# Kernel tuning notes

Measured on AMD Instinct MI355X. Metric: run time of the kernel, lower is better.

Reference implementation:

```python
import jax, jax.numpy as jnp
import numpy as np

BN_EPS = 1e-3  # Keras BatchNormalization default epsilon

def setup_inputs() -> dict:
    key = jax.random.key(0)
    ks = jax.random.split(key, 6)
    B, H, W, C = 8, 128, 128, 128
    s = 0.05  # small init scale for weights
    return {
        "x1": jax.random.normal(ks[0], (B, H, W, C), jnp.float32),
        "x2": jax.random.normal(ks[1], (B, H, W, C), jnp.float32),
        "Wq": jax.random.normal(ks[2], (C, C), jnp.float32) * s,
        "Wk": jax.random.normal(ks[3], (C, C), jnp.float32) * s,
        "Wv": jax.random.normal(ks[4], (C, C), jnp.float32) * s,
        "Ws": jax.random.normal(ks[5], (C, C), jnp.float32) * s,
        "bs": jnp.zeros((C,), jnp.float32),
        "scale": jnp.ones((1,), jnp.float32),   # layers.Attention use_scale=True, init 1
        "gamma": jnp.ones((C,), jnp.float32),
        "beta": jnp.zeros((C,), jnp.float32),
        "mu": jnp.zeros((C,), jnp.float32),
        "var": jnp.ones((C,), jnp.float32),
    }


def reference(x1, x2, Wq, Wk, Wv, Ws, bs, scale, gamma, beta, mu, var):
    # x1, x2: [B,H,W,C].  1x1 convs with relu == per-pixel channel matmul.
    q = jax.nn.relu(jnp.einsum('bhwc,cd->bhwd', x1, Wq))  # [B,H,W,C]
    k = jax.nn.relu(jnp.einsum('bhwc,cd->bhwd', x1, Wk))
    v = jax.nn.relu(jnp.einsum('bhwc,cd->bhwd', x2, Wv))
    # After transpose [0,3,1,2], Keras Attention batches over (B,C):
    # seq axis = H (rows), feature dim = W (cols). Fold the transposes into einsum.
    scores = scale[0] * jnp.einsum('bhwc,bgwc->bchg', q, k)  # [B,C,H,H]
    attn = jax.nn.softmax(scores, axis=-1)
    # attn @ v over row axis g, then implicit transpose back to NHWC.
    o = jnp.einsum('bchg,bgwc->bhwc', attn, v)  # [B,H,W,C]
    # sigmoid 1x1 conv (with bias), then inference-mode BatchNorm.
    g = jax.nn.sigmoid(jnp.einsum('bhwc,cd->bhwd', o, Ws) + bs)
    g = gamma * (g - mu) * jax.lax.rsqrt(var + BN_EPS) + beta
    # gated residual
    return x1 + x2 * g
```

## Files before the change

### kernel.cpp

```cpp
#include <hip/hip_runtime.h>

typedef unsigned int u32;
typedef unsigned short u16;
typedef u16 u16x4 __attribute__((ext_vector_type(4)));
typedef u16 u16x8 __attribute__((ext_vector_type(8)));
typedef __bf16 bf16x8 __attribute__((ext_vector_type(8)));
typedef float f32x4 __attribute__((ext_vector_type(4)));

#define LDK 136
#define MFMA(a, b, c) __builtin_amdgcn_mfma_f32_16x16x32_bf16(a, b, c, 0, 0, 0)

__device__ __forceinline__ u16 f2b(float f) {
  u32 u = __builtin_bit_cast(u32, f);
  u = (u + 0x7fffu + ((u >> 16) & 1u)) >> 16;
  return (u16)u;
}
__device__ __forceinline__ float b2f(u16 h) {
  u32 u = ((u32)h) << 16;
  return __builtin_bit_cast(float, u);
}

__global__ void wprep(const float* __restrict__ Wq, const float* __restrict__ Wk,
                      const float* __restrict__ Wv, const float* __restrict__ Ws,
                      u16* __restrict__ wT) {
  const float* srcs[4] = {Wq, Wk, Wv, Ws};
  const float* s = srcs[blockIdx.x];
  u16* d = wT + (size_t)blockIdx.x * 16384;
  for (int idx = threadIdx.x; idx < 16384; idx += 256) {
    int i = idx >> 7, j = idx & 127;
    d[j * 128 + i] = f2b(s[idx]);
  }
}

__global__ __launch_bounds__(256, 2)
void qkv_kernel(const float* __restrict__ x1, const float* __restrict__ x2,
                const u16* __restrict__ wT,
                u16* __restrict__ q_t, u16* __restrict__ k_t, u16* __restrict__ v_t) {
  __shared__ u16 Xs[128 * LDK];
  __shared__ u16 ST[128 * LDK];

  const int t = threadIdx.x;
  const int bh = blockIdx.x;
  const int b = bh >> 7, h = bh & 127;
  const size_t pixbase = (size_t)bh * 16384;
  const size_t obase = (size_t)b * 2097152 + (size_t)h * 128;

#pragma unroll
  for (int j = 0; j < 8; ++j) {
    int lin = j * 256 + t;
    int w = lin >> 4, c0 = (lin & 15) << 3;
    f32x4 a0 = *(const f32x4*)&x1[pixbase + lin * 8];
    f32x4 a1 = *(const f32x4*)&x1[pixbase + lin * 8 + 4];
    u16x8 p;
#pragma unroll
    for (int i = 0; i < 4; ++i) { p[i] = f2b(a0[i]); p[4 + i] = f2b(a1[i]); }
    *(u16x8*)&Xs[w * LDK + c0] = p;
  }
  __syncthreads();

  const int lane = t & 63, wave = t >> 6;
  const int lrow = lane & 15, lq = lane >> 4;
  const int nstrip = wave * 32;

  u16* outs[3] = {q_t, k_t, v_t};

  for (int m = 0; m < 3; ++m) {
    const u16* wb = wT + (size_t)m * 16384;
    bf16x8 w0[4], w1[4];
#pragma unroll
    for (int kk = 0; kk < 4; ++kk) {
      int ko = kk * 32 + lq * 8;
      w0[kk] = *(const bf16x8*)&wb[(nstrip + lrow) * 128 + ko];
      w1[kk] = *(const bf16x8*)&wb[(nstrip + 16 + lrow) * 128 + ko];
    }

    if (m == 2) {
#pragma unroll
      for (int j = 0; j < 8; ++j) {
        int lin = j * 256 + t;
        int w = lin >> 4, c0 = (lin & 15) << 3;
        f32x4 a0 = *(const f32x4*)&x2[pixbase + lin * 8];
        f32x4 a1 = *(const f32x4*)&x2[pixbase + lin * 8 + 4];
        u16x8 p;
#pragma unroll
        for (int i = 0; i < 4; ++i) { p[i] = f2b(a0[i]); p[4 + i] = f2b(a1[i]); }
        *(u16x8*)&Xs[w * LDK + c0] = p;
      }
      __syncthreads();
    }

    f32x4 acc[8][2];
#pragma unroll
    for (int mt = 0; mt < 8; ++mt) {
      acc[mt][0] = (f32x4){0.f, 0.f, 0.f, 0.f};
      acc[mt][1] = (f32x4){0.f, 0.f, 0.f, 0.f};
    }
#pragma unroll
    for (int kk = 0; kk < 4; ++kk) {
      int ko = kk * 32 + lq * 8;
#pragma unroll
      for (int mt = 0; mt < 8; ++mt) {
        bf16x8 a = *(const bf16x8*)&Xs[(mt * 16 + lrow) * LDK + ko];
        acc[mt][0] = MFMA(a, w0[kk], acc[mt][0]);
        acc[mt][1] = MFMA(a, w1[kk], acc[mt][1]);
      }
    }
    __syncthreads();

#pragma unroll
    for (int mt = 0; mt < 8; ++mt) {
      int w0i = mt * 16 + lq * 4;
#pragma unroll
      for (int nt = 0; nt < 2; ++nt) {
        int c = nstrip + nt * 16 + lrow;
        u16x4 p;
#pragma unroll
        for (int r = 0; r < 4; ++r) p[r] = f2b(fmaxf(acc[mt][nt][r], 0.f));
        *(u16x4*)&ST[c * LDK + w0i] = p;
      }
    }
    __syncthreads();

    u16* dst = outs[m];
    {
      int c = t >> 1, w0i = (t & 1) * 64;
#pragma unroll
      for (int j = 0; j < 8; ++j)
        *(u16x8*)&dst[obase + (size_t)c * 16384 + w0i + j * 8] =
            *(const u16x8*)&ST[c * LDK + w0i + j * 8];
    }
  }
}

__global__ __launch_bounds__(256, 2)
void attn_kernel(u16* __restrict__ q_t, const u16* __restrict__ k_t,
                 const u16* __restrict__ v_t, const float* __restrict__ scale_p) {
  __shared__ u16 Ks[128 * LDK];
  __shared__ u16 QP[128 * LDK];

  const int t = threadIdx.x;
  const size_t base = (size_t)blockIdx.x * 16384;

#pragma unroll
  for (int j = 0; j < 8; ++j) {
    int lin = j * 256 + t;
    int r = lin >> 4, c0 = (lin & 15) << 3;
    *(u16x8*)&QP[r * LDK + c0] = *(const u16x8*)&q_t[base + lin * 8];
    *(u16x8*)&Ks[r * LDK + c0] = *(const u16x8*)&k_t[base + lin * 8];
  }
  __syncthreads();

  const int lane = t & 63, wave = t >> 6;
  const int lrow = lane & 15, lq = lane >> 4;
  const int hstrip = wave * 32;
  const float scl = scale_p[0];

  f32x4 acc[8][2];
#pragma unroll
  for (int mt = 0; mt < 8; ++mt) {
    acc[mt][0] = (f32x4){0.f, 0.f, 0.f, 0.f};
    acc[mt][1] = (f32x4){0.f, 0.f, 0.f, 0.f};
  }
#pragma unroll
  for (int kk = 0; kk < 4; ++kk) {
    int ko = kk * 32 + lq * 8;
    bf16x8 b0 = *(const bf16x8*)&QP[(hstrip + lrow) * LDK + ko];
    bf16x8 b1 = *(const bf16x8*)&QP[(hstrip + 16 + lrow) * LDK + ko];
#pragma unroll
    for (int mt = 0; mt < 8; ++mt) {
      bf16x8 a = *(const bf16x8*)&Ks[(mt * 16 + lrow) * LDK + ko];
      acc[mt][0] = MFMA(a, b0, acc[mt][0]);
      acc[mt][1] = MFMA(a, b1, acc[mt][1]);
    }
  }

  const int g0 = (t & 15) * 8, w0v = (t >> 4) * 8;
  u16x8 vv[8];
#pragma unroll
  for (int i = 0; i < 8; ++i)
    vv[i] = *(const u16x8*)&v_t[base + (g0 + i) * 128 + w0v];

  float inv[2];
#pragma unroll
  for (int nt = 0; nt < 2; ++nt) {
    float mx = -1e30f;
#pragma unroll
    for (int mt = 0; mt < 8; ++mt)
#pragma unroll
      for (int r = 0; r < 4; ++r) {
        acc[mt][nt][r] *= scl;
        mx = fmaxf(mx, acc[mt][nt][r]);
      }
    mx = fmaxf(mx, __shfl_xor(mx, 16));
    mx = fmaxf(mx, __shfl_xor(mx, 32));
    float s = 0.f;
#pragma unroll
    for (int mt = 0; mt < 8; ++mt)
#pragma unroll
      for (int r = 0; r < 4; ++r) {
        float e = __expf(acc[mt][nt][r] - mx);
        acc[mt][nt][r] = e;
        s += e;
      }
    s += __shfl_xor(s, 16);
    s += __shfl_xor(s, 32);
    inv[nt] = 1.f / s;
  }
  __syncthreads();

#pragma unroll
  for (int j = 0; j < 8; ++j) {
    u16x8 tv;
#pragma unroll
    for (int i = 0; i < 8; ++i) tv[i] = vv[i][j];
    *(u16x8*)&Ks[(w0v + j) * LDK + g0] = tv;
  }
#pragma unroll
  for (int mt = 0; mt < 8; ++mt) {
    int gg0 = mt * 16 + lq * 4;
#pragma unroll
    for (int nt = 0; nt < 2; ++nt) {
      int hh = hstrip + nt * 16 + lrow;
      u16x4 p;
#pragma unroll
      for (int r = 0; r < 4; ++r) p[r] = f2b(acc[mt][nt][r] * inv[nt]);
      *(u16x4*)&QP[hh * LDK + gg0] = p;
    }
  }
  __syncthreads();

  f32x4 o[8][2];
#pragma unroll
  for (int mt = 0; mt < 8; ++mt) {
    o[mt][0] = (f32x4){0.f, 0.f, 0.f, 0.f};
    o[mt][1] = (f32x4){0.f, 0.f, 0.f, 0.f};
  }
#pragma unroll
  for (int kk = 0; kk < 4; ++kk) {
    int ko = kk * 32 + lq * 8;
    bf16x8 b0 = *(const bf16x8*)&QP[(hstrip + lrow) * LDK + ko];
    bf16x8 b1 = *(const bf16x8*)&QP[(hstrip + 16 + lrow) * LDK + ko];
#pragma unroll
    for (int mt = 0; mt < 8; ++mt) {
      bf16x8 a = *(const bf16x8*)&Ks[(mt * 16 + lrow) * LDK + ko];
      o[mt][0] = MFMA(a, b0, o[mt][0]);
      o[mt][1] = MFMA(a, b1, o[mt][1]);
    }
  }
  __syncthreads();

#pragma unroll
  for (int mt = 0; mt < 8; ++mt) {
    int w0i = mt * 16 + lq * 4;
#pragma unroll
    for (int nt = 0; nt < 2; ++nt) {
      int hh = hstrip + nt * 16 + lrow;
      u16x4 p;
#pragma unroll
      for (int r = 0; r < 4; ++r) p[r] = f2b(o[mt][nt][r]);
      *(u16x4*)&Ks[hh * LDK + w0i] = p;
    }
  }
  __syncthreads();

  {
    int hh = t >> 1, w0i = (t & 1) * 64;
#pragma unroll
    for (int j = 0; j < 8; ++j)
      *(u16x8*)&q_t[base + hh * 128 + w0i + j * 8] =
          *(const u16x8*)&Ks[hh * LDK + w0i + j * 8];
  }
}

__global__ __launch_bounds__(256, 3)
void final_kernel(const u16* __restrict__ o_t, const u16* __restrict__ wsT,
                  const float* __restrict__ x1, const float* __restrict__ x2,
                  const float* __restrict__ bs, const float* __restrict__ gamma,
                  const float* __restrict__ beta, const float* __restrict__ mu,
                  const float* __restrict__ var, float* __restrict__ out) {
  __shared__ u16 Os[128 * LDK];
  __shared__ float bnA[128], bnB[128], bsf[128];

  const int t = threadIdx.x;
  const int bh = blockIdx.x;
  const int b = bh >> 7, h = bh & 127;
  const size_t obase = (size_t)b * 2097152 + (size_t)h * 128;
  const size_t pixbase = (size_t)bh * 16384;

  if (t < 128) {
    float a = gamma[t] * rsqrtf(var[t] + 1e-3f);
    bnA[t] = a;
    bnB[t] = beta[t] - mu[t] * a;
    bsf[t] = bs[t];
  }
  {
    int c0 = (t & 15) * 8, w0 = (t >> 4) * 8;
    u16 ov[8][8];
#pragma unroll
    for (int i = 0; i < 8; ++i)
      *(u16x8*)&ov[i][0] = *(const u16x8*)&o_t[obase + (size_t)(c0 + i) * 16384 + w0];
#pragma unroll
    for (int j = 0; j < 8; ++j) {
      u16x8 tv;
#pragma unroll
      for (int i = 0; i < 8; ++i) tv[i] = ov[i][j];
      *(u16x8*)&Os[(w0 + j) * LDK + c0] = tv;
    }
  }
  __syncthreads();

  const int lane = t & 63, wave = t >> 6;
  const int lrow = lane & 15, lq = lane >> 4;
  const int wstrip = wave * 32;

  f32x4 acc[8][2];
#pragma unroll
  for (int mt = 0; mt < 8; ++mt) {
    acc[mt][0] = (f32x4){0.f, 0.f, 0.f, 0.f};
    acc[mt][1] = (f32x4){0.f, 0.f, 0.f, 0.f};
  }
#pragma unroll
  for (int kk = 0; kk < 4; ++kk) {
    int ko = kk * 32 + lq * 8;
    bf16x8 b0 = *(const bf16x8*)&Os[(wstrip + lrow) * LDK + ko];
    bf16x8 b1 = *(const bf16x8*)&Os[(wstrip + 16 + lrow) * LDK + ko];
#pragma unroll
    for (int mt = 0; mt < 8; ++mt) {
      bf16x8 a = *(const bf16x8*)&wsT[(mt * 16 + lrow) * 128 + ko];
      acc[mt][0] = MFMA(a, b0, acc[mt][0]);
      acc[mt][1] = MFMA(a, b1, acc[mt][1]);
    }
  }
  __syncthreads();

#pragma unroll
  for (int mt = 0; mt < 8; ++mt) {
    int d0 = mt * 16 + lq * 4;
#pragma unroll
    for (int nt = 0; nt < 2; ++nt) {
      int w = wstrip + nt * 16 + lrow;
      u16x4 p;
#pragma unroll
      for (int r = 0; r < 4; ++r) {
        int d = d0 + r;
        float sv = acc[mt][nt][r] + bsf[d];
        float sg = 1.f / (1.f + __expf(-sv));
        p[r] = f2b(bnA[d] * sg + bnB[d]);
      }
      *(u16x4*)&Os[w * LDK + d0] = p;
    }
  }
  __syncthreads();

  {
    int w = t >> 1, d0 = (t & 1) * 64;
#pragma unroll
    for (int j = 0; j < 8; ++j) {
      int d = d0 + j * 8;
      u16x8 g8 = *(const u16x8*)&Os[w * LDK + d];
      f32x4 a0 = *(const f32x4*)&x1[pixbase + w * 128 + d];
      f32x4 a1 = *(const f32x4*)&x1[pixbase + w * 128 + d + 4];
      f32x4 c0v = *(const f32x4*)&x2[pixbase + w * 128 + d];
      f32x4 c1v = *(const f32x4*)&x2[pixbase + w * 128 + d + 4];
      f32x4 r0, r1;
#pragma unroll
      for (int i = 0; i < 4; ++i) {
        r0[i] = a0[i] + c0v[i] * b2f(g8[i]);
        r1[i] = a1[i] + c1v[i] * b2f(g8[4 + i]);
      }
      *(f32x4*)&out[pixbase + w * 128 + d] = r0;
      *(f32x4*)&out[pixbase + w * 128 + d + 4] = r1;
    }
  }
}

extern "C" void kernel_launch(void* const* d_in, const int* in_sizes, int n_in,
                              void* d_out, int out_size, void* d_ws, size_t ws_size,
                              hipStream_t stream) {
  const float* x1 = (const float*)d_in[0];
  const float* x2 = (const float*)d_in[1];
  const float* Wq = (const float*)d_in[2];
  const float* Wk = (const float*)d_in[3];
  const float* Wv = (const float*)d_in[4];
  const float* Ws = (const float*)d_in[5];
  const float* bs = (const float*)d_in[6];
  const float* scale = (const float*)d_in[7];
  const float* gamma = (const float*)d_in[8];
  const float* beta = (const float*)d_in[9];
  const float* mu = (const float*)d_in[10];
  const float* var = (const float*)d_in[11];
  float* outp = (float*)d_out;

  u16* q_t = (u16*)d_ws;
  u16* k_t = q_t + 16777216;
  u16* v_t = k_t + 16777216;
  u16* wT = v_t + 16777216;

  wprep<<<dim3(4), dim3(256), 0, stream>>>(Wq, Wk, Wv, Ws, wT);
  qkv_kernel<<<dim3(1024), dim3(256), 0, stream>>>(x1, x2, wT, q_t, k_t, v_t);
  attn_kernel<<<dim3(1024), dim3(256), 0, stream>>>(q_t, k_t, v_t, scale);
  final_kernel<<<dim3(1024), dim3(256), 0, stream>>>(q_t, wT + 3 * 16384, x1, x2, bs,
                                                     gamma, beta, mu, var, outp);
}
```

Baseline: 360.9 us.

## Split QKV projection across grid Y and cut shared-memory staging in attention

```diff
diff --git a/kernel.cpp b/kernel.cpp
--- a/kernel.cpp
+++ b/kernel.cpp
@@ -32,25 +32,41 @@
   }
 }
 
-__global__ __launch_bounds__(256, 2)
+__global__ __launch_bounds__(256, 4)
 void qkv_kernel(const float* __restrict__ x1, const float* __restrict__ x2,
                 const u16* __restrict__ wT,
                 u16* __restrict__ q_t, u16* __restrict__ k_t, u16* __restrict__ v_t) {
   __shared__ u16 Xs[128 * LDK];
-  __shared__ u16 ST[128 * LDK];
 
   const int t = threadIdx.x;
   const int bh = blockIdx.x;
+  const int m = blockIdx.y;
   const int b = bh >> 7, h = bh & 127;
   const size_t pixbase = (size_t)bh * 16384;
   const size_t obase = (size_t)b * 2097152 + (size_t)h * 128;
 
+  const float* xin = (m == 2) ? x2 : x1;
+  u16* dst = (m == 0) ? q_t : (m == 1) ? k_t : v_t;
+
+  const int lane = t & 63, wave = t >> 6;
+  const int lrow = lane & 15, lq = lane >> 4;
+  const int nstrip = wave * 32;
+
+  const u16* wb = wT + (size_t)m * 16384;
+  bf16x8 w0[4], w1[4];
+#pragma unroll
+  for (int kk = 0; kk < 4; ++kk) {
+    int ko = kk * 32 + lq * 8;
+    w0[kk] = *(const bf16x8*)&wb[(nstrip + lrow) * 128 + ko];
+    w1[kk] = *(const bf16x8*)&wb[(nstrip + 16 + lrow) * 128 + ko];
+  }
+
 #pragma unroll
   for (int j = 0; j < 8; ++j) {
     int lin = j * 256 + t;
     int w = lin >> 4, c0 = (lin & 15) << 3;
-    f32x4 a0 = *(const f32x4*)&x1[pixbase + lin * 8];
-    f32x4 a1 = *(const f32x4*)&x1[pixbase + lin * 8 + 4];
+    f32x4 a0 = *(const f32x4*)&xin[pixbase + lin * 8];
+    f32x4 a1 = *(const f32x4*)&xin[pixbase + lin * 8 + 4];
     u16x8 p;
 #pragma unroll
     for (int i = 0; i < 4; ++i) { p[i] = f2b(a0[i]); p[4 + i] = f2b(a1[i]); }
@@ -58,76 +74,33 @@
   }
   __syncthreads();
 
-  const int lane = t & 63, wave = t >> 6;
-  const int lrow = lane & 15, lq = lane >> 4;
-  const int nstrip = wave * 32;
-
-  u16* outs[3] = {q_t, k_t, v_t};
-
-  for (int m = 0; m < 3; ++m) {
-    const u16* wb = wT + (size_t)m * 16384;
-    bf16x8 w0[4], w1[4];
-#pragma unroll
-    for (int kk = 0; kk < 4; ++kk) {
-      int ko = kk * 32 + lq * 8;
-      w0[kk] = *(const bf16x8*)&wb[(nstrip + lrow) * 128 + ko];
-      w1[kk] = *(const bf16x8*)&wb[(nstrip + 16 + lrow) * 128 + ko];
-    }
-
-    if (m == 2) {
-#pragma unroll
-      for (int j = 0; j < 8; ++j) {
-        int lin = j * 256 + t;
-        int w = lin >> 4, c0 = (lin & 15) << 3;
-        f32x4 a0 = *(const f32x4*)&x2[pixbase + lin * 8];
-        f32x4 a1 = *(const f32x4*)&x2[pixbase + lin * 8 + 4];
-        u16x8 p;
-#pragma unroll
-        for (int i = 0; i < 4; ++i) { p[i] = f2b(a0[i]); p[4 + i] = f2b(a1[i]); }
-        *(u16x8*)&Xs[w * LDK + c0] = p;
-      }
-      __syncthreads();
-    }
-
-    f32x4 acc[8][2];
+  f32x4 acc[8][2];
+#pragma unroll
+  for (int mt = 0; mt < 8; ++mt) {
+    acc[mt][0] = (f32x4){0.f, 0.f, 0.f, 0.f};
+    acc[mt][1] = (f32x4){0.f, 0.f, 0.f, 0.f};
+  }
+#pragma unroll
+  for (int kk = 0; kk < 4; ++kk) {
+    int ko = kk * 32 + lq * 8;
 #pragma unroll
     for (int mt = 0; mt < 8; ++mt) {
-      acc[mt][0] = (f32x4){0.f, 0.f, 0.f, 0.f};
-      acc[mt][1] = (f32x4){0.f, 0.f, 0.f, 0.f};
-    }
-#pragma unroll
-    for (int kk = 0; kk < 4; ++kk) {
-      int ko = kk * 32 + lq * 8;
-#pragma unroll
-      for (int mt = 0; mt < 8; ++mt) {
-        bf16x8 a = *(const bf16x8*)&Xs[(mt * 16 + lrow) * LDK + ko];
-        acc[mt][0] = MFMA(a, w0[kk], acc[mt][0]);
-        acc[mt][1] = MFMA(a, w1[kk], acc[mt][1]);
-      }
-    }
-    __syncthreads();
-
-#pragma unroll
-    for (int mt = 0; mt < 8; ++mt) {
-      int w0i = mt * 16 + lq * 4;
-#pragma unroll
-      for (int nt = 0; nt < 2; ++nt) {
-        int c = nstrip + nt * 16 + lrow;
-        u16x4 p;
-#pragma unroll
-        for (int r = 0; r < 4; ++r) p[r] = f2b(fmaxf(acc[mt][nt][r], 0.f));
-        *(u16x4*)&ST[c * LDK + w0i] = p;
-      }
-    }
-    __syncthreads();
-
-    u16* dst = outs[m];
-    {
-      int c = t >> 1, w0i = (t & 1) * 64;
-#pragma unroll
-      for (int j = 0; j < 8; ++j)
-        *(u16x8*)&dst[obase + (size_t)c * 16384 + w0i + j * 8] =
-            *(const u16x8*)&ST[c * LDK + w0i + j * 8];
+      bf16x8 a = *(const bf16x8*)&Xs[(mt * 16 + lrow) * LDK + ko];
+      acc[mt][0] = MFMA(a, w0[kk], acc[mt][0]);
+      acc[mt][1] = MFMA(a, w1[kk], acc[mt][1]);
+    }
+  }
+
+#pragma unroll
+  for (int mt = 0; mt < 8; ++mt) {
+    int w0i = mt * 16 + lq * 4;
+#pragma unroll
+    for (int nt = 0; nt < 2; ++nt) {
+      int c = nstrip + nt * 16 + lrow;
+      u16x4 p;
+#pragma unroll
+      for (int r = 0; r < 4; ++r) p[r] = f2b(fmaxf(acc[mt][nt][r], 0.f));
+      *(u16x4*)&dst[obase + (size_t)c * 16384 + w0i] = p;
     }
   }
 }
@@ -136,25 +109,36 @@
 void attn_kernel(u16* __restrict__ q_t, const u16* __restrict__ k_t,
                  const u16* __restrict__ v_t, const float* __restrict__ scale_p) {
   __shared__ u16 Ks[128 * LDK];
-  __shared__ u16 QP[128 * LDK];
+  __shared__ u16 Ps[128 * LDK];
 
   const int t = threadIdx.x;
   const size_t base = (size_t)blockIdx.x * 16384;
-
-#pragma unroll
-  for (int j = 0; j < 8; ++j) {
-    int lin = j * 256 + t;
-    int r = lin >> 4, c0 = (lin & 15) << 3;
-    *(u16x8*)&QP[r * LDK + c0] = *(const u16x8*)&q_t[base + lin * 8];
-    *(u16x8*)&Ks[r * LDK + c0] = *(const u16x8*)&k_t[base + lin * 8];
-  }
-  __syncthreads();
 
   const int lane = t & 63, wave = t >> 6;
   const int lrow = lane & 15, lq = lane >> 4;
   const int hstrip = wave * 32;
   const float scl = scale_p[0];
 
+  bf16x8 q0[4], q1[4];
+#pragma unroll
+  for (int kk = 0; kk < 4; ++kk) {
+    int ko = kk * 32 + lq * 8;
+    q0[kk] = *(const bf16x8*)&q_t[base + (hstrip + lrow) * 128 + ko];
+    q1[kk] = *(const bf16x8*)&q_t[base + (hstrip + 16 + lrow) * 128 + ko];
+  }
+  const int g0 = (t & 15) * 8, w0v = (t >> 4) * 8;
+  u16x8 vv[8];
+#pragma unroll
+  for (int i = 0; i < 8; ++i)
+    vv[i] = *(const u16x8*)&v_t[base + (g0 + i) * 128 + w0v];
+#pragma unroll
+  for (int j = 0; j < 8; ++j) {
+    int lin = j * 256 + t;
+    int r = lin >> 4, c0 = (lin & 15) << 3;
+    *(u16x8*)&Ks[r * LDK + c0] = *(const u16x8*)&k_t[base + lin * 8];
+  }
+  __syncthreads();
+
   f32x4 acc[8][2];
 #pragma unroll
   for (int mt = 0; mt < 8; ++mt) {
@@ -164,8 +148,75 @@
 #pragma unroll
   for (int kk = 0; kk < 4; ++kk) {
     int ko = kk * 32 + lq * 8;
-    bf16x8 b0 = *(const bf16x8*)&QP[(hstrip + lrow) * LDK + ko];
-    bf16x8 b1 = *(const bf16x8*)&QP[(hstrip + 16 + lrow) * LDK + ko];
+#pragma unroll
+    for (int mt = 0; mt < 8; ++mt) {
+      bf16x8 a = *(const bf16x8*)&Ks[(mt * 16 + lrow) * LDK + ko];
+      acc[mt][0] = MFMA(a, q0[kk], acc[mt][0]);
+      acc[mt][1] = MFMA(a, q1[kk], acc[mt][1]);
+    }
+  }
+
+  float inv[2];
+#pragma unroll
+  for (int nt = 0; nt < 2; ++nt) {
+    float mx = -1e30f;
+#pragma unroll
+    for (int mt = 0; mt < 8; ++mt)
+#pragma unroll
+      for (int r = 0; r < 4; ++r) {
+        acc[mt][nt][r] *= scl;
+        mx = fmaxf(mx, acc[mt][nt][r]);
+      }
+    mx = fmaxf(mx, __shfl_xor(mx, 16));
+    mx = fmaxf(mx, __shfl_xor(mx, 32));
+    float s = 0.f;
+#pragma unroll
+    for (int mt = 0; mt < 8; ++mt)
+#pragma unroll
+      for (int r = 0; r < 4; ++r) {
+        float e = __expf(acc[mt][nt][r] - mx);
+        acc[mt][nt][r] = e;
+        s += e;
+      }
+    s += __shfl_xor(s, 16);
+    s += __shfl_xor(s, 32);
+    inv[nt] = 1.f / s;
+  }
+  __syncthreads();
+
+#pragma unroll
+  for (int j = 0; j < 8; ++j) {
+    u16x8 tv;
+#pragma unroll
+    for (int i = 0; i < 8; ++i) tv[i] = vv[i][j];
+    *(u16x8*)&Ks[(w0v + j) * LDK + g0] = tv;
+  }
+#pragma unroll
+  for (int mt = 0; mt < 8; ++mt) {
+    int gg0 = mt * 16 + lq * 4;
+#pragma unroll
+    for (int nt = 0; nt < 2; ++nt) {
+      int hh = hstrip + nt * 16 + lrow;
+      u16x4 p;
+#pragma unroll
+      for (int r = 0; r < 4; ++r) p[r] = f2b(acc[mt][nt][r] * inv[nt]);
+      *(u16x4*)&Ps[hh * LDK + gg0] = p;
+    }
+  }
+  __syncthreads();
+
+#pragma unroll
+  for (int kk = 0; kk < 4; ++kk) {
+    int ko = kk * 32 + lq * 8;
+    bf16x8 b0 = *(const bf16x8*)&Ps[(hstrip + lrow) * LDK + ko];
+    bf16x8 b1 = *(const bf16x8*)&Ps[(hstrip + 16 + lrow) * LDK + ko];
+    if (kk == 0) {
+#pragma unroll
+      for (int mt = 0; mt < 8; ++mt) {
+        acc[mt][0] = (f32x4){0.f, 0.f, 0.f, 0.f};
+        acc[mt][1] = (f32x4){0.f, 0.f, 0.f, 0.f};
+      }
+    }
 #pragma unroll
     for (int mt = 0; mt < 8; ++mt) {
       bf16x8 a = *(const bf16x8*)&Ks[(mt * 16 + lrow) * LDK + ko];
@@ -173,106 +224,21 @@
       acc[mt][1] = MFMA(a, b1, acc[mt][1]);
     }
   }
-
-  const int g0 = (t & 15) * 8, w0v = (t >> 4) * 8;
-  u16x8 vv[8];
-#pragma unroll
-  for (int i = 0; i < 8; ++i)
-    vv[i] = *(const u16x8*)&v_t[base + (g0 + i) * 128 + w0v];
-
-  float inv[2];
-#pragma unroll
-  for (int nt = 0; nt < 2; ++nt) {
-    float mx = -1e30f;
-#pragma unroll
-    for (int mt = 0; mt < 8; ++mt)
-#pragma unroll
-      for (int r = 0; r < 4; ++r) {
-        acc[mt][nt][r] *= scl;
-        mx = fmaxf(mx, acc[mt][nt][r]);
-      }
-    mx = fmaxf(mx, __shfl_xor(mx, 16));
-    mx = fmaxf(mx, __shfl_xor(mx, 32));
-    float s = 0.f;
-#pragma unroll
-    for (int mt = 0; mt < 8; ++mt)
-#pragma unroll
-      for (int r = 0; r < 4; ++r) {
-        float e = __expf(acc[mt][nt][r] - mx);
-        acc[mt][nt][r] = e;
-        s += e;
-      }
-    s += __shfl_xor(s, 16);
-    s += __shfl_xor(s, 32);
-    inv[nt] = 1.f / s;
-  }
-  __syncthreads();
-
-#pragma unroll
-  for (int j = 0; j < 8; ++j) {
-    u16x8 tv;
-#pragma unroll
-    for (int i = 0; i < 8; ++i) tv[i] = vv[i][j];
-    *(u16x8*)&Ks[(w0v + j) * LDK + g0] = tv;
-  }
-#pragma unroll
-  for (int mt = 0; mt < 8; ++mt) {
-    int gg0 = mt * 16 + lq * 4;
+#pragma unroll
+  for (int mt = 0; mt < 8; ++mt) {
+    int w0i = mt * 16 + lq * 4;
 #pragma unroll
     for (int nt = 0; nt < 2; ++nt) {
       int hh = hstrip + nt * 16 + lrow;
       u16x4 p;
 #pragma unroll
-      for (int r = 0; r < 4; ++r) p[r] = f2b(acc[mt][nt][r] * inv[nt]);
-      *(u16x4*)&QP[hh * LDK + gg0] = p;
-    }
-  }
-  __syncthreads();
-
-  f32x4 o[8][2];
-#pragma unroll
-  for (int mt = 0; mt < 8; ++mt) {
-    o[mt][0] = (f32x4){0.f, 0.f, 0.f, 0.f};
-    o[mt][1] = (f32x4){0.f, 0.f, 0.f, 0.f};
-  }
-#pragma unroll
-  for (int kk = 0; kk < 4; ++kk) {
-    int ko = kk * 32 + lq * 8;
-    bf16x8 b0 = *(const bf16x8*)&QP[(hstrip + lrow) * LDK + ko];
-    bf16x8 b1 = *(const bf16x8*)&QP[(hstrip + 16 + lrow) * LDK + ko];
-#pragma unroll
-    for (int mt = 0; mt < 8; ++mt) {
-      bf16x8 a = *(const bf16x8*)&Ks[(mt * 16 + lrow) * LDK + ko];
-      o[mt][0] = MFMA(a, b0, o[mt][0]);
-      o[mt][1] = MFMA(a, b1, o[mt][1]);
-    }
-  }
-  __syncthreads();
-
-#pragma unroll
-  for (int mt = 0; mt < 8; ++mt) {
-    int w0i = mt * 16 + lq * 4;
-#pragma unroll
-    for (int nt = 0; nt < 2; ++nt) {
-      int hh = hstrip + nt * 16 + lrow;
-      u16x4 p;
-#pragma unroll
-      for (int r = 0; r < 4; ++r) p[r] = f2b(o[mt][nt][r]);
-      *(u16x4*)&Ks[hh * LDK + w0i] = p;
-    }
-  }
-  __syncthreads();
-
-  {
-    int hh = t >> 1, w0i = (t & 1) * 64;
-#pragma unroll
-    for (int j = 0; j < 8; ++j)
-      *(u16x8*)&q_t[base + hh * 128 + w0i + j * 8] =
-          *(const u16x8*)&Ks[hh * LDK + w0i + j * 8];
-  }
-}
-
-__global__ __launch_bounds__(256, 3)
+      for (int r = 0; r < 4; ++r) p[r] = f2b(acc[mt][nt][r]);
+      *(u16x4*)&q_t[base + hh * 128 + w0i] = p;
+    }
+  }
+}
+
+__global__ __launch_bounds__(256, 4)
 void final_kernel(const u16* __restrict__ o_t, const u16* __restrict__ wsT,
                   const float* __restrict__ x1, const float* __restrict__ x2,
                   const float* __restrict__ bs, const float* __restrict__ gamma,
@@ -397,7 +363,7 @@
   u16* wT = v_t + 16777216;
 
   wprep<<<dim3(4), dim3(256), 0, stream>>>(Wq, Wk, Wv, Ws, wT);
-  qkv_kernel<<<dim3(1024), dim3(256), 0, stream>>>(x1, x2, wT, q_t, k_t, v_t);
+  qkv_kernel<<<dim3(1024, 3), dim3(256), 0, stream>>>(x1, x2, wT, q_t, k_t, v_t);
   attn_kernel<<<dim3(1024), dim3(256), 0, stream>>>(q_t, k_t, v_t, scale);
   final_kernel<<<dim3(1024), dim3(256), 0, stream>>>(q_t, wT + 3 * 16384, x1, x2, bs,
                                                      gamma, beta, mu, var, outp);
```

New measurement: 346.4 us. 1.04x faster.
